# Kernel optimization log

Hardware: AMD Instinct MI355X
Metric: run time of the kernel (lower is better)

## Reference

```python
import jax, jax.numpy as jnp
import numpy as np

N_NODES = 100000
N_EDGES = 1600000
N_GRAPHS = 64
IN_DIM = 128
HID = 64
N_CLASSES = 10


def setup_inputs() -> dict:
    key = jax.random.key(0)
    ks = jax.random.split(key, 8)
    x = jax.random.normal(ks[0], (N_NODES, IN_DIM), jnp.float32)
    edge_index = jax.random.randint(ks[1], (2, N_EDGES), 0, N_NODES, jnp.int32)
    graph_id = jnp.sort(jax.random.randint(ks[2], (N_NODES,), 0, N_GRAPHS, jnp.int32))
    W1 = jax.random.normal(ks[3], (IN_DIM, HID), jnp.float32) / np.sqrt(IN_DIM)
    b1 = jnp.zeros((HID,), jnp.float32)
    W2 = jax.random.normal(ks[4], (HID, HID), jnp.float32) / np.sqrt(HID)
    b2 = jnp.zeros((HID,), jnp.float32)
    attn_W = jax.random.normal(ks[5], (HID, 1), jnp.float32) / np.sqrt(HID)
    attn_b = jnp.zeros((1,), jnp.float32)
    cls_W = jax.random.normal(ks[6], (HID, N_CLASSES), jnp.float32) / np.sqrt(HID)
    cls_b = jnp.zeros((N_CLASSES,), jnp.float32)
    return {"x": x, "edge_index": edge_index, "graph_id": graph_id,
            "W1": W1, "b1": b1, "W2": W2, "b2": b2,
            "attn_W": attn_W, "attn_b": attn_b, "cls_W": cls_W, "cls_b": cls_b}


def _graph_conv(h, W, b, src, dst, norm_out, norm_in):
    # DGL GraphConv, norm='both': D_in^{-1/2} A D_out^{-1/2} (h W) + b
    h = h @ W                                  # [N, out]
    h = h * norm_out[:, None]                  # scale by src out-degree^{-1/2}
    m = jax.ops.segment_sum(h[src], dst, num_segments=N_NODES)  # SpMM aggregation
    return m * norm_in[:, None] + b


def reference(x, edge_index, graph_id, W1, b1, W2, b2, attn_W, attn_b, cls_W, cls_b):
    src, dst = edge_index[0], edge_index[1]
    ones_e = jnp.ones((src.shape[0],), jnp.float32)
    deg_out = jnp.clip(jax.ops.segment_sum(ones_e, src, num_segments=N_NODES), 1.0)
    deg_in = jnp.clip(jax.ops.segment_sum(ones_e, dst, num_segments=N_NODES), 1.0)
    norm_out = jax.lax.rsqrt(deg_out)
    norm_in = jax.lax.rsqrt(deg_in)

    h = jax.nn.relu(_graph_conv(x, W1, b1, src, dst, norm_out, norm_in))
    h = jax.nn.relu(_graph_conv(h, W2, b2, src, dst, norm_out, norm_in))

    hw = jax.nn.sigmoid(h @ attn_W + attn_b)   # [N, 1] attention gate
    h = h * hw

    # mean_nodes: per-graph mean pooling
    sums = jax.ops.segment_sum(h, graph_id, num_segments=N_GRAPHS)        # [G, HID]
    cnts = jnp.clip(jax.ops.segment_sum(jnp.ones((N_NODES,), jnp.float32), graph_id,
                                        num_segments=N_GRAPHS), 1.0)
    hg = sums / cnts[:, None]
    out = hg @ cls_W + cls_b                   # [G, n_classes]
    return out, hw
```

## Files before the change

### kernel.cpp

```cpp
#include <hip/hip_runtime.h>
#include <stdint.h>


#define N_NODES   100000
#define N_EDGES   1600000
#define N_GRAPHS  64
#define IN_DIM    128
#define HID       64
#define N_CLASSES 10

#define NBUCK     391
#define P1B       196
#define EPB       8192
#define GB_BLOCKS 391
#define MTILES    6250
#define GEMM_BLOCKS 1563
#define SPMM_BLOCKS 3125
#define POOL_SLICES 32
#define WS_NEED   33885952u

typedef __attribute__((ext_vector_type(8))) short short8v;
typedef __attribute__((ext_vector_type(4))) float f32x4;
typedef __bf16 bf16x8 __attribute__((ext_vector_type(8)));

__device__ __forceinline__ f32x4 mfma16(short8v a, short8v b, f32x4 c) {
  return __builtin_amdgcn_mfma_f32_16x16x32_bf16(
      __builtin_bit_cast(bf16x8, a), __builtin_bit_cast(bf16x8, b), c, 0, 0, 0);
}

__device__ __forceinline__ float bf2f(unsigned short u) {
  unsigned int v = ((unsigned int)u) << 16;
  float f;
  __builtin_memcpy(&f, &v, 4);
  return f;
}

__device__ __forceinline__ unsigned short f2bf(float f) {
  unsigned int x;
  __builtin_memcpy(&x, &f, 4);
  unsigned int lsb = (x >> 16) & 1u;
  x += 0x7fffu + lsb;
  return (unsigned short)(x >> 16);
}

__device__ __forceinline__ void unpack_bf2(unsigned int u, float& lo, float& hi) {
  unsigned int a = u << 16;
  unsigned int b = u & 0xffff0000u;
  __builtin_memcpy(&lo, &a, 4);
  __builtin_memcpy(&hi, &b, 4);
}

__device__ __forceinline__ float ldf(const void* p, int i, int mode) {
  return mode ? bf2f(((const unsigned short*)p)[i]) : ((const float*)p)[i];
}

__global__ __launch_bounds__(256) void probe_kernel(const unsigned short* __restrict__ xu,
                                                    int* __restrict__ flag) {
  int tid = (int)threadIdx.x;
  unsigned u = xu[2 * tid];
  int e = (int)((u >> 7) & 0xFF);
  int ok = (e >= 110 && e <= 132) ? 1 : 0;
  unsigned long long m = __ballot(ok);
  __shared__ int cnt[4];
  if ((tid & 63) == 0) cnt[tid >> 6] = __popcll(m);
  __syncthreads();
  if (tid == 0) {
    flag[0] = (cnt[0] + cnt[1] + cnt[2] + cnt[3] > 128) ? 1 : 0;
    flag[1] = 1;
  }
}

__global__ __launch_bounds__(256) void fallback_kernel(unsigned short* __restrict__ out,
                                                       int n) {
  int i = blockIdx.x * 256 + threadIdx.x;
  if (i < n) out[i] = 0;
}

__global__ __launch_bounds__(256) void wcvt_kernel(
    const void* __restrict__ W1, const void* __restrict__ W2,
    const void* __restrict__ b1, const void* __restrict__ b2,
    const void* __restrict__ attnW, const void* __restrict__ attnb,
    const void* __restrict__ clsW, const void* __restrict__ clsb,
    unsigned short* __restrict__ W1hf, unsigned short* __restrict__ W1lf,
    unsigned short* __restrict__ W2hf, unsigned short* __restrict__ W2lf,
    float* __restrict__ b1f, float* __restrict__ b2f,
    float* __restrict__ attnWf, float* __restrict__ attnbf,
    float* __restrict__ clsWf, float* __restrict__ clsbf,
    const int* __restrict__ flag) {
  int mode = flag[0];
  int i = blockIdx.x * 256 + threadIdx.x;
  if (i < 1024) {
    int tile = i >> 6, lane = i & 63;
    int kt = tile >> 2, ct = tile & 3;
#pragma unroll
    for (int j = 0; j < 8; ++j) {
      int k = kt * 32 + ((lane >> 4) << 3) + j;
      int d = (ct << 4) + (lane & 15);
      float v = ldf(W1, k * HID + d, mode);
      unsigned short h = f2bf(v);
      unsigned short l = f2bf(v - bf2f(h));
      W1hf[i * 8 + j] = h;
      W1lf[i * 8 + j] = l;
    }
  } else if (i < 1536) {
    int ii = i - 1024;
    int tile = ii >> 6, lane = ii & 63;
    int kt = tile >> 2, ct = tile & 3;
#pragma unroll
    for (int j = 0; j < 8; ++j) {
      int k = kt * 32 + ((lane >> 4) << 3) + j;
      int d = (ct << 4) + (lane & 15);
      float v = ldf(W2, k * HID + d, mode);
      unsigned short h = f2bf(v);
      unsigned short l = f2bf(v - bf2f(h));
      W2hf[ii * 8 + j] = h;
      W2lf[ii * 8 + j] = l;
    }
  }
  if (i < HID) {
    b1f[i] = ldf(b1, i, mode);
    b2f[i] = ldf(b2, i, mode);
    attnWf[i] = ldf(attnW, i, mode);
  }
  if (i == 0) attnbf[0] = ldf(attnb, 0, mode);
  if (i < HID * N_CLASSES) clsWf[i] = ldf(clsW, i, mode);
  if (i < N_CLASSES) clsbf[i] = ldf(clsb, i, mode);
}

__global__ __launch_bounds__(256) void part_count_kernel(
    const int* __restrict__ ei, int* __restrict__ blkhistD,
    int* __restrict__ blkhistS,
    const int* __restrict__ gid, int* __restrict__ gstart) {
  int b = (int)blockIdx.x;
  int t = (int)threadIdx.x;
  if (b < P1B) {
    __shared__ int hD[NBUCK];
    __shared__ int hS[NBUCK];
    for (int i = t; i < NBUCK; i += 256) { hD[i] = 0; hS[i] = 0; }
    __syncthreads();
    int base_e = b * EPB;
    for (int s = 0; s < EPB / 1024; ++s) {
      int e4 = base_e + s * 1024 + t * 4;
      if (e4 < N_EDGES) {
        int4 s4 = *(const int4*)(ei + e4);
        int4 d4 = *(const int4*)(ei + N_EDGES + e4);
        int ss[4] = {s4.x, s4.y, s4.z, s4.w};
        int dd[4] = {d4.x, d4.y, d4.z, d4.w};
#pragma unroll
        for (int j = 0; j < 4; ++j) {
          if ((unsigned)ss[j] < N_NODES) atomicAdd(&hS[ss[j] >> 8], 1);
          if ((unsigned)dd[j] < N_NODES) atomicAdd(&hD[dd[j] >> 8], 1);
        }
      }
    }
    __syncthreads();
    for (int i = t; i < NBUCK; i += 256) {
      blkhistD[b * NBUCK + i] = hD[i];
      blkhistS[b * NBUCK + i] = hS[i];
    }
  } else {
    int bb = b - P1B;
    int n = bb * 256 + t;
    if (n >= N_NODES) return;
    int gc = gid[n] & (N_GRAPHS - 1);
    if (n == 0) {
      for (int g = 0; g <= gc; ++g) gstart[g] = 0;
    } else {
      int gp = gid[n - 1] & (N_GRAPHS - 1);
      for (int g = gp + 1; g <= gc; ++g) gstart[g] = n;
    }
    if (n == N_NODES - 1) {
      for (int g = gc + 1; g <= N_GRAPHS; ++g) gstart[g] = N_NODES;
    }
  }
}

__global__ __launch_bounds__(512) void bucket_scan_kernel(
    int* __restrict__ blkhistD, int* __restrict__ blkhistS,
    int* __restrict__ bstart_d, int* __restrict__ bstart_s) {
  int* hist = (blockIdx.x == 0) ? blkhistD : blkhistS;
  int* bst  = (blockIdx.x == 0) ? bstart_d : bstart_s;
  int u = (int)threadIdx.x;
  int tot = 0;
  if (u < NBUCK) {
    for (int blk = 0; blk < P1B; ++blk) tot += hist[blk * NBUCK + u];
  }
  __shared__ int smA[512];
  __shared__ int smB[512];
  smA[u] = tot;
  __syncthreads();
  int* a = smA;
  int* bq = smB;
  for (int off = 1; off < 512; off <<= 1) {
    int v = a[u];
    if (u >= off) v += a[u - off];
    bq[u] = v;
    __syncthreads();
    int* tmp = a; a = bq; bq = tmp;
  }
  int excl = a[u] - tot;
  if (u <= NBUCK) bst[u] = excl;
  if (u < NBUCK) {
    int off2 = excl;
    for (int blk = 0; blk < P1B; ++blk) {
      int h = hist[blk * NBUCK + u];
      hist[blk * NBUCK + u] = off2;
      off2 += h;
    }
  }
}

__global__ __launch_bounds__(256) void part_scatter_kernel(
    const int* __restrict__ ei, const int* __restrict__ blkbaseD,
    const int* __restrict__ blkbaseS,
    int2* __restrict__ edst, int* __restrict__ esrc) {
  __shared__ int cD[NBUCK];
  __shared__ int cS[NBUCK];
  int b = (int)blockIdx.x;
  int t = (int)threadIdx.x;
  for (int i = t; i < NBUCK; i += 256) {
    cD[i] = blkbaseD[b * NBUCK + i];
    cS[i] = blkbaseS[b * NBUCK + i];
  }
  __syncthreads();
  int base_e = b * EPB;
  for (int s = 0; s < EPB / 1024; ++s) {
    int e4 = base_e + s * 1024 + t * 4;
    if (e4 < N_EDGES) {
      int4 s4 = *(const int4*)(ei + e4);
      int4 d4 = *(const int4*)(ei + N_EDGES + e4);
      int ss[4] = {s4.x, s4.y, s4.z, s4.w};
      int dd[4] = {d4.x, d4.y, d4.z, d4.w};
#pragma unroll
      for (int j = 0; j < 4; ++j) {
        if ((unsigned)ss[j] < N_NODES) {
          int slot = atomicAdd(&cS[ss[j] >> 8], 1);
          esrc[slot] = ss[j];
        }
        if ((unsigned)dd[j] < N_NODES) {
          int slot = atomicAdd(&cD[dd[j] >> 8], 1);
          edst[slot] = make_int2(ss[j], dd[j]);
        }
      }
    }
  }
}

__global__ __launch_bounds__(256) void csr_kernel(
    const int2* __restrict__ edst, const int* __restrict__ esrc,
    const int* __restrict__ bstart_d, const int* __restrict__ bstart_s,
    int* __restrict__ rowptr, int* __restrict__ colx,
    float* __restrict__ norm_in, float* __restrict__ norm_out) {
  __shared__ int lc[256];
  __shared__ int smA[256];
  __shared__ int smB[256];
  int b = (int)blockIdx.x;
  int t = (int)threadIdx.x;
  if (b < NBUCK) {
    int node0 = b << 8;
    int base = bstart_d[b];
    int end  = bstart_d[b + 1];
    lc[t] = 0;
    __syncthreads();
    for (int i = base + t; i < end; i += 256) {
      int2 p = edst[i];
      atomicAdd(&lc[p.y - node0], 1);
    }
    __syncthreads();
    int my = lc[t];
    smA[t] = my;
    __syncthreads();
    int* a = smA;
    int* bq = smB;
    for (int off = 1; off < 256; off <<= 1) {
      int v = a[t];
      if (t >= off) v += a[t - off];
      bq[t] = v;
      __syncthreads();
      int* tmp = a; a = bq; bq = tmp;
    }
    int excl = a[t] - my;
    int n = node0 + t;
    if (n <= N_NODES) rowptr[n] = base + excl;
    if (n < N_NODES) {
      int c = my < 1 ? 1 : my;
      norm_in[n] = rsqrtf((float)c);
    }
    __syncthreads();
    lc[t] = base + excl;
    __syncthreads();
    for (int i = base + t; i < end; i += 256) {
      int2 p = edst[i];
      int slot = atomicAdd(&lc[p.y - node0], 1);
      colx[slot] = p.x;
    }
  } else {
    int bb = b - NBUCK;
    int node0 = bb << 8;
    int base = bstart_s[bb];
    int end  = bstart_s[bb + 1];
    lc[t] = 0;
    __syncthreads();
    for (int i = base + t; i < end; i += 256) {
      atomicAdd(&lc[esrc[i] - node0], 1);
    }
    __syncthreads();
    int n = node0 + t;
    if (n < N_NODES) {
      int c = lc[t] < 1 ? 1 : lc[t];
      norm_out[n] = rsqrtf((float)c);
    }
  }
}

template <int K>
__global__ __launch_bounds__(256) void gemm_mfma_kernel(
    const void* __restrict__ A, const unsigned short* __restrict__ Whf,
    const unsigned short* __restrict__ Wlf, const float* __restrict__ norm_out,
    unsigned short* __restrict__ out, const int* __restrict__ flag) {
  int mode = flag[0];
  int mtile = (int)blockIdx.x * 4 + ((int)threadIdx.x >> 6);
  if (mtile >= MTILES) return;
  int n0 = mtile << 4;
  int lane = (int)threadIdx.x & 63;
  int row = lane & 15;
  int kg = lane >> 4;
  f32x4 acc0 = {0.f, 0.f, 0.f, 0.f};
  f32x4 acc1 = {0.f, 0.f, 0.f, 0.f};
  f32x4 acc2 = {0.f, 0.f, 0.f, 0.f};
  f32x4 acc3 = {0.f, 0.f, 0.f, 0.f};
  const short8v* whb0 = (const short8v*)Whf + lane;
  const short8v* wlb0 = (const short8v*)Wlf + lane;
  if (mode) {
    const unsigned short* xr = (const unsigned short*)A + (size_t)(n0 + row) * K + (kg << 3);
#pragma unroll
    for (int kt = 0; kt < K / 32; ++kt) {
      uint4 va = *(const uint4*)(xr + kt * 32);
      short8v xh = __builtin_bit_cast(short8v, va);
      const short8v* wh = whb0 + (size_t)(kt * 4) * 64;
      const short8v* wl = wlb0 + (size_t)(kt * 4) * 64;
      acc0 = mfma16(xh, wh[0], acc0);
      acc1 = mfma16(xh, wh[64], acc1);
      acc2 = mfma16(xh, wh[128], acc2);
      acc3 = mfma16(xh, wh[192], acc3);
      acc0 = mfma16(xh, wl[0], acc0);
      acc1 = mfma16(xh, wl[64], acc1);
      acc2 = mfma16(xh, wl[128], acc2);
      acc3 = mfma16(xh, wl[192], acc3);
    }
  } else {
    const float* xr = (const float*)A + (size_t)(n0 + row) * K + (kg << 3);
#pragma unroll
    for (int kt = 0; kt < K / 32; ++kt) {
      float4 a0 = *(const float4*)(xr + kt * 32);
      float4 a1 = *(const float4*)(xr + kt * 32 + 4);
      float xv[8] = {a0.x, a0.y, a0.z, a0.w, a1.x, a1.y, a1.z, a1.w};
      short8v xh, xl;
#pragma unroll
      for (int j = 0; j < 8; ++j) {
        unsigned short h = f2bf(xv[j]);
        unsigned short l = f2bf(xv[j] - bf2f(h));
        xh[j] = (short)h;
        xl[j] = (short)l;
      }
      const short8v* wh = whb0 + (size_t)(kt * 4) * 64;
      const short8v* wl = wlb0 + (size_t)(kt * 4) * 64;
      acc0 = mfma16(xh, wh[0], acc0);
      acc1 = mfma16(xh, wh[64], acc1);
      acc2 = mfma16(xh, wh[128], acc2);
      acc3 = mfma16(xh, wh[192], acc3);
      acc0 = mfma16(xh, wl[0], acc0);
      acc1 = mfma16(xh, wl[64], acc1);
      acc2 = mfma16(xh, wl[128], acc2);
      acc3 = mfma16(xh, wl[192], acc3);
      acc0 = mfma16(xl, wh[0], acc0);
      acc1 = mfma16(xl, wh[64], acc1);
      acc2 = mfma16(xl, wh[128], acc2);
      acc3 = mfma16(xl, wh[192], acc3);
    }
  }
  int col = lane & 15;
#pragma unroll
  for (int i = 0; i < 4; ++i) {
    int n = n0 + (kg << 2) + i;
    float s = norm_out[n];
    size_t rb = (size_t)n << 6;
    out[rb + col]      = f2bf(acc0[i] * s);
    out[rb + 16 + col] = f2bf(acc1[i] * s);
    out[rb + 32 + col] = f2bf(acc2[i] * s);
    out[rb + 48 + col] = f2bf(acc3[i] * s);
  }
}

__device__ __forceinline__ void accum8(uint4 v, float acc[8]) {
  float lo, hi;
  unpack_bf2(v.x, lo, hi); acc[0] += lo; acc[1] += hi;
  unpack_bf2(v.y, lo, hi); acc[2] += lo; acc[3] += hi;
  unpack_bf2(v.z, lo, hi); acc[4] += lo; acc[5] += hi;
  unpack_bf2(v.w, lo, hi); acc[6] += lo; acc[7] += hi;
}

__device__ __forceinline__ void spmm_gather8(const unsigned short* __restrict__ hs,
                                             const int* __restrict__ col,
                                             int e0, int e1, int dim0,
                                             float acc[8]) {
  int e = e0;
  for (; e + 4 <= e1; e += 4) {
    unsigned c0 = (unsigned)col[e];
    unsigned c1 = (unsigned)col[e + 1];
    unsigned c2 = (unsigned)col[e + 2];
    unsigned c3 = (unsigned)col[e + 3];
    uint4 v0 = make_uint4(0u, 0u, 0u, 0u);
    uint4 v1 = v0, v2 = v0, v3 = v0;
    if (c0 < N_NODES) v0 = *(const uint4*)(hs + ((size_t)c0 << 6) + dim0);
    if (c1 < N_NODES) v1 = *(const uint4*)(hs + ((size_t)c1 << 6) + dim0);
    if (c2 < N_NODES) v2 = *(const uint4*)(hs + ((size_t)c2 << 6) + dim0);
    if (c3 < N_NODES) v3 = *(const uint4*)(hs + ((size_t)c3 << 6) + dim0);
    accum8(v0, acc);
    accum8(v1, acc);
    accum8(v2, acc);
    accum8(v3, acc);
  }
  for (; e < e1; ++e) {
    unsigned c = (unsigned)col[e];
    uint4 v = make_uint4(0u, 0u, 0u, 0u);
    if (c < N_NODES) v = *(const uint4*)(hs + ((size_t)c << 6) + dim0);
    accum8(v, acc);
  }
}

__global__ __launch_bounds__(256) void spmm_kernel(const unsigned short* __restrict__ hs,
                                                   const int* __restrict__ rowptr,
                                                   const int* __restrict__ col,
                                                   const float* __restrict__ norm_in,
                                                   const float* __restrict__ b1f,
                                                   unsigned short* __restrict__ out) {
  int n = (int)(blockIdx.x * 32 + (threadIdx.x >> 3));
  int dim0 = ((int)threadIdx.x & 7) << 3;
  if (n >= N_NODES) return;
  int e0 = rowptr[n], e1 = rowptr[n + 1];
  if (e0 < 0) e0 = 0;
  if (e1 > N_EDGES) e1 = N_EDGES;
  float acc[8];
#pragma unroll
  for (int i = 0; i < 8; ++i) acc[i] = 0.f;
  spmm_gather8(hs, col, e0, e1, dim0, acc);
  float nin = norm_in[n];
  unsigned int pk[4];
#pragma unroll
  for (int i = 0; i < 4; ++i) {
    float vlo = fmaxf(acc[2 * i] * nin + b1f[dim0 + 2 * i], 0.f);
    float vhi = fmaxf(acc[2 * i + 1] * nin + b1f[dim0 + 2 * i + 1], 0.f);
    pk[i] = (unsigned int)f2bf(vlo) | ((unsigned int)f2bf(vhi) << 16);
  }
  *(uint4*)(out + ((size_t)n << 6) + dim0) = make_uint4(pk[0], pk[1], pk[2], pk[3]);
}

__global__ __launch_bounds__(256) void spmm_attn_kernel(
    const unsigned short* __restrict__ hs,
    const int* __restrict__ rowptr, const int* __restrict__ col,
    const float* __restrict__ norm_in, const float* __restrict__ b2f,
    const float* __restrict__ attnWf, const float* __restrict__ attnbf,
    void* __restrict__ out_base, unsigned short* __restrict__ gated,
    const int* __restrict__ flag) {
  int mode = flag[0];
  int n = (int)(blockIdx.x * 32 + (threadIdx.x >> 3));
  int dim0 = ((int)threadIdx.x & 7) << 3;
  if (n >= N_NODES) return;
  int e0 = rowptr[n], e1 = rowptr[n + 1];
  if (e0 < 0) e0 = 0;
  if (e1 > N_EDGES) e1 = N_EDGES;
  float acc[8];
#pragma unroll
  for (int i = 0; i < 8; ++i) acc[i] = 0.f;
  spmm_gather8(hs, col, e0, e1, dim0, acc);
  float nin = norm_in[n];
  float vv[8];
  float p = 0.f;
#pragma unroll
  for (int i = 0; i < 8; ++i) {
    vv[i] = fmaxf(acc[i] * nin + b2f[dim0 + i], 0.f);
    p += vv[i] * attnWf[dim0 + i];
  }
#pragma unroll
  for (int m = 1; m <= 4; m <<= 1) p += __shfl_xor(p, m, 64);
  float logit = p + attnbf[0];
  float hwv = 1.f / (1.f + __expf(-logit));
  if ((threadIdx.x & 7) == 0) {
    if (mode) ((unsigned short*)out_base)[N_GRAPHS * N_CLASSES + n] = f2bf(hwv);
    else      ((float*)out_base)[N_GRAPHS * N_CLASSES + n] = hwv;
  }
  unsigned int pk[4];
#pragma unroll
  for (int i = 0; i < 4; ++i) {
    pk[i] = (unsigned int)f2bf(vv[2 * i] * hwv) |
            ((unsigned int)f2bf(vv[2 * i + 1] * hwv) << 16);
  }
  *(uint4*)(gated + ((size_t)n << 6) + dim0) = make_uint4(pk[0], pk[1], pk[2], pk[3]);
}

__global__ __launch_bounds__(256) void pool_kernel(const unsigned short* __restrict__ gated,
                                                   const int* __restrict__ gstart,
                                                   float* __restrict__ gpart) {
  int g = (int)blockIdx.x >> 5;
  int s = (int)blockIdx.x & 31;
  int dim = (int)threadIdx.x & 63;
  int rsel = (int)threadIdx.x >> 6;
  int r0 = gstart[g], r1 = gstart[g + 1];
  if (r0 < 0) r0 = 0;
  if (r1 > N_NODES) r1 = N_NODES;
  int len = r1 - r0;
  if (len < 0) len = 0;
  int a = r0 + (int)(((long long)len * s) >> 5);
  int bnd = r0 + (int)(((long long)len * (s + 1)) >> 5);
  float acc = 0.f;
  for (int r = a + rsel; r < bnd; r += 4)
    acc += bf2f(gated[((size_t)r << 6) + dim]);
  __shared__ float sm[256];
  sm[threadIdx.x] = acc;
  __syncthreads();
  if (threadIdx.x < 64)
    gpart[((size_t)blockIdx.x << 6) + dim] =
        sm[dim] + sm[64 + dim] + sm[128 + dim] + sm[192 + dim];
}

__global__ __launch_bounds__(64) void pool_reduce_kernel(const float* __restrict__ gpart,
                                                         float* __restrict__ gsum) {
  int g = (int)blockIdx.x;
  int dim = (int)threadIdx.x;
  float acc = 0.f;
#pragma unroll
  for (int s = 0; s < POOL_SLICES; ++s)
    acc += gpart[(((size_t)g << 5) + s << 6) + dim];
  gsum[((size_t)g << 6) + dim] = acc;
}

__global__ __launch_bounds__(640) void final_kernel(const float* __restrict__ gsum,
                                                    const int* __restrict__ gstart,
                                                    const float* __restrict__ clsWf,
                                                    const float* __restrict__ clsbf,
                                                    void* __restrict__ out_base,
                                                    const int* __restrict__ flag) {
  int mode = flag[0];
  int t = (int)threadIdx.x;
  if (t >= N_GRAPHS * N_CLASSES) return;
  int g = t / N_CLASSES, c = t - g * N_CLASSES;
  int cg = gstart[g + 1] - gstart[g];
  if (cg < 1) cg = 1;
  float inv = 1.f / (float)cg;
  float acc = 0.f;
#pragma unroll
  for (int d = 0; d < HID; ++d) acc += gsum[(g << 6) + d] * clsWf[d * N_CLASSES + c];
  float r = acc * inv + clsbf[c];
  if (mode) ((unsigned short*)out_base)[t] = f2bf(r);
  else      ((float*)out_base)[t] = r;
}

extern "C" void kernel_launch(void* const* d_in, const int* in_sizes, int n_in,
                              void* d_out, int out_size, void* d_ws, size_t ws_size,
                              hipStream_t stream) {
  const void* x     = d_in[0];
  const int*  ei    = (const int*)d_in[1];
  const int*  gid   = (const int*)d_in[2];
  const void* W1    = d_in[3];
  const void* b1    = d_in[4];
  const void* W2    = d_in[5];
  const void* b2    = d_in[6];
  const void* attnW = d_in[7];
  const void* attnb = d_in[8];
  const void* clsW  = d_in[9];
  const void* clsb  = d_in[10];

  if (ws_size < (size_t)WS_NEED) {
    fallback_kernel<<<(out_size + 255) / 256, 256, 0, stream>>>(
        (unsigned short*)d_out, out_size);
    return;
  }

  char* w = (char*)d_ws;
  int*   flag     = (int*)(w + 0);
  int*   gstart   = (int*)(w + 64);
  float* gsum     = (float*)(w + 576);
  int*   bstart_d = (int*)(w + 16960);
  int*   bstart_s = (int*)(w + 18560);
  int*   blkhD    = (int*)(w + 20160);
  int*   blkhS    = (int*)(w + 326720);
  int*   rowptr   = (int*)(w + 633280);
  float* norm_out = (float*)(w + 1033344);
  float* norm_in  = (float*)(w + 1433344);
  unsigned short* W1hf = (unsigned short*)(w + 1833344);
  unsigned short* W1lf = (unsigned short*)(w + 1849728);
  unsigned short* W2hf = (unsigned short*)(w + 1866112);
  unsigned short* W2lf = (unsigned short*)(w + 1874304);
  float* b1f      = (float*)(w + 1882496);
  float* b2f      = (float*)(w + 1882752);
  float* attnWf   = (float*)(w + 1883008);
  float* attnbf   = (float*)(w + 1883264);
  float* clsWf    = (float*)(w + 1883328);
  float* clsbf    = (float*)(w + 1885888);
  int*   colx     = (int*)(w + 1885952);
  int2*  edst     = (int2*)(w + 8285952);
  int*   esrc     = (int*)(w + 21085952);
  unsigned short* bufA = (unsigned short*)(w + 8285952);
  unsigned short* bufB = (unsigned short*)(w + 21085952);
  float* gpart    = (float*)(w + 20160);

  probe_kernel<<<1, 256, 0, stream>>>((const unsigned short*)x, flag);
  wcvt_kernel<<<32, 256, 0, stream>>>(W1, W2, b1, b2, attnW, attnb, clsW, clsb,
                                      W1hf, W1lf, W2hf, W2lf, b1f, b2f, attnWf,
                                      attnbf, clsWf, clsbf, flag);

  part_count_kernel<<<P1B + GB_BLOCKS, 256, 0, stream>>>(ei, blkhD, blkhS, gid, gstart);
  bucket_scan_kernel<<<2, 512, 0, stream>>>(blkhD, blkhS, bstart_d, bstart_s);
  part_scatter_kernel<<<P1B, 256, 0, stream>>>(ei, blkhD, blkhS, edst, esrc);
  csr_kernel<<<2 * NBUCK, 256, 0, stream>>>(edst, esrc, bstart_d, bstart_s,
                                            rowptr, colx, norm_in, norm_out);

  gemm_mfma_kernel<IN_DIM><<<GEMM_BLOCKS, 256, 0, stream>>>(
      x, W1hf, W1lf, norm_out, bufA, flag);
  spmm_kernel<<<SPMM_BLOCKS, 256, 0, stream>>>(bufA, rowptr, colx, norm_in, b1f, bufB);

  gemm_mfma_kernel<HID><<<GEMM_BLOCKS, 256, 0, stream>>>(
      bufB, W2hf, W2lf, norm_out, bufA, flag + 1);
  spmm_attn_kernel<<<SPMM_BLOCKS, 256, 0, stream>>>(
      bufA, rowptr, colx, norm_in, b2f, attnWf, attnbf, d_out, bufB, flag);

  pool_kernel<<<N_GRAPHS * POOL_SLICES, 256, 0, stream>>>(bufB, gstart, gpart);
  pool_reduce_kernel<<<N_GRAPHS, 64, 0, stream>>>(gpart, gsum);
  final_kernel<<<1, 640, 0, stream>>>(gsum, gstart, clsWf, clsbf, d_out, flag);
}
```

Measured before the change: 274.7 us.

## Fuse probe into weight conversion and overlap layer-1 GEMM with edge histogram

Folds the dtype probe into the weight-conversion kernel, and merges the layer-1 GEMM into the histogram/graph-start kernel. This is possible because the norm_out scaling moves from the GEMM epilogue into the first SpMM gather. Edge-destination pairs are packed into 32-bit words to cut CSR build traffic, and the pool reduction is folded into the final classifier kernel. These changes remove several launches and let the dense GEMM run alongside the partitioning work. In exchange, the first SpMM does an extra per-edge norm_out load and buffer aliasing gets more involved.

After: 270.0 us. No clear change (-1.7%).

```diff
diff --git a/kernel.cpp b/kernel.cpp
--- a/kernel.cpp
+++ b/kernel.cpp
@@ -54,22 +54,6 @@
   return mode ? bf2f(((const unsigned short*)p)[i]) : ((const float*)p)[i];
 }
 
-__global__ __launch_bounds__(256) void probe_kernel(const unsigned short* __restrict__ xu,
-                                                    int* __restrict__ flag) {
-  int tid = (int)threadIdx.x;
-  unsigned u = xu[2 * tid];
-  int e = (int)((u >> 7) & 0xFF);
-  int ok = (e >= 110 && e <= 132) ? 1 : 0;
-  unsigned long long m = __ballot(ok);
-  __shared__ int cnt[4];
-  if ((tid & 63) == 0) cnt[tid >> 6] = __popcll(m);
-  __syncthreads();
-  if (tid == 0) {
-    flag[0] = (cnt[0] + cnt[1] + cnt[2] + cnt[3] > 128) ? 1 : 0;
-    flag[1] = 1;
-  }
-}
-
 __global__ __launch_bounds__(256) void fallback_kernel(unsigned short* __restrict__ out,
                                                        int n) {
   int i = blockIdx.x * 256 + threadIdx.x;
@@ -77,6 +61,7 @@
 }
 
 __global__ __launch_bounds__(256) void wcvt_kernel(
+    const unsigned short* __restrict__ xu,
     const void* __restrict__ W1, const void* __restrict__ W2,
     const void* __restrict__ b1, const void* __restrict__ b2,
     const void* __restrict__ attnW, const void* __restrict__ attnb,
@@ -86,9 +71,27 @@
     float* __restrict__ b1f, float* __restrict__ b2f,
     float* __restrict__ attnWf, float* __restrict__ attnbf,
     float* __restrict__ clsWf, float* __restrict__ clsbf,
-    const int* __restrict__ flag) {
-  int mode = flag[0];
-  int i = blockIdx.x * 256 + threadIdx.x;
+    int* __restrict__ flag) {
+  __shared__ int cnt[4];
+  __shared__ int smode;
+  int tid = (int)threadIdx.x;
+  unsigned u = xu[2 * tid];
+  int e = (int)((u >> 7) & 0xFF);
+  int ok = (e >= 110 && e <= 132) ? 1 : 0;
+  unsigned long long m = __ballot(ok);
+  if ((tid & 63) == 0) cnt[tid >> 6] = __popcll(m);
+  __syncthreads();
+  if (tid == 0) {
+    smode = (cnt[0] + cnt[1] + cnt[2] + cnt[3] > 128) ? 1 : 0;
+    if (blockIdx.x == 0) {
+      flag[0] = smode;
+      flag[1] = 1;
+    }
+  }
+  __syncthreads();
+  int mode = smode;
+
+  int i = blockIdx.x * 256 + tid;
   if (i < 1024) {
     int tile = i >> 6, lane = i & 63;
     int kt = tile >> 2, ct = tile & 3;
@@ -127,202 +130,12 @@
   if (i < N_CLASSES) clsbf[i] = ldf(clsb, i, mode);
 }
 
-__global__ __launch_bounds__(256) void part_count_kernel(
-    const int* __restrict__ ei, int* __restrict__ blkhistD,
-    int* __restrict__ blkhistS,
-    const int* __restrict__ gid, int* __restrict__ gstart) {
-  int b = (int)blockIdx.x;
-  int t = (int)threadIdx.x;
-  if (b < P1B) {
-    __shared__ int hD[NBUCK];
-    __shared__ int hS[NBUCK];
-    for (int i = t; i < NBUCK; i += 256) { hD[i] = 0; hS[i] = 0; }
-    __syncthreads();
-    int base_e = b * EPB;
-    for (int s = 0; s < EPB / 1024; ++s) {
-      int e4 = base_e + s * 1024 + t * 4;
-      if (e4 < N_EDGES) {
-        int4 s4 = *(const int4*)(ei + e4);
-        int4 d4 = *(const int4*)(ei + N_EDGES + e4);
-        int ss[4] = {s4.x, s4.y, s4.z, s4.w};
-        int dd[4] = {d4.x, d4.y, d4.z, d4.w};
-#pragma unroll
-        for (int j = 0; j < 4; ++j) {
-          if ((unsigned)ss[j] < N_NODES) atomicAdd(&hS[ss[j] >> 8], 1);
-          if ((unsigned)dd[j] < N_NODES) atomicAdd(&hD[dd[j] >> 8], 1);
-        }
-      }
-    }
-    __syncthreads();
-    for (int i = t; i < NBUCK; i += 256) {
-      blkhistD[b * NBUCK + i] = hD[i];
-      blkhistS[b * NBUCK + i] = hS[i];
-    }
-  } else {
-    int bb = b - P1B;
-    int n = bb * 256 + t;
-    if (n >= N_NODES) return;
-    int gc = gid[n] & (N_GRAPHS - 1);
-    if (n == 0) {
-      for (int g = 0; g <= gc; ++g) gstart[g] = 0;
-    } else {
-      int gp = gid[n - 1] & (N_GRAPHS - 1);
-      for (int g = gp + 1; g <= gc; ++g) gstart[g] = n;
-    }
-    if (n == N_NODES - 1) {
-      for (int g = gc + 1; g <= N_GRAPHS; ++g) gstart[g] = N_NODES;
-    }
-  }
-}
-
-__global__ __launch_bounds__(512) void bucket_scan_kernel(
-    int* __restrict__ blkhistD, int* __restrict__ blkhistS,
-    int* __restrict__ bstart_d, int* __restrict__ bstart_s) {
-  int* hist = (blockIdx.x == 0) ? blkhistD : blkhistS;
-  int* bst  = (blockIdx.x == 0) ? bstart_d : bstart_s;
-  int u = (int)threadIdx.x;
-  int tot = 0;
-  if (u < NBUCK) {
-    for (int blk = 0; blk < P1B; ++blk) tot += hist[blk * NBUCK + u];
-  }
-  __shared__ int smA[512];
-  __shared__ int smB[512];
-  smA[u] = tot;
-  __syncthreads();
-  int* a = smA;
-  int* bq = smB;
-  for (int off = 1; off < 512; off <<= 1) {
-    int v = a[u];
-    if (u >= off) v += a[u - off];
-    bq[u] = v;
-    __syncthreads();
-    int* tmp = a; a = bq; bq = tmp;
-  }
-  int excl = a[u] - tot;
-  if (u <= NBUCK) bst[u] = excl;
-  if (u < NBUCK) {
-    int off2 = excl;
-    for (int blk = 0; blk < P1B; ++blk) {
-      int h = hist[blk * NBUCK + u];
-      hist[blk * NBUCK + u] = off2;
-      off2 += h;
-    }
-  }
-}
-
-__global__ __launch_bounds__(256) void part_scatter_kernel(
-    const int* __restrict__ ei, const int* __restrict__ blkbaseD,
-    const int* __restrict__ blkbaseS,
-    int2* __restrict__ edst, int* __restrict__ esrc) {
-  __shared__ int cD[NBUCK];
-  __shared__ int cS[NBUCK];
-  int b = (int)blockIdx.x;
-  int t = (int)threadIdx.x;
-  for (int i = t; i < NBUCK; i += 256) {
-    cD[i] = blkbaseD[b * NBUCK + i];
-    cS[i] = blkbaseS[b * NBUCK + i];
-  }
-  __syncthreads();
-  int base_e = b * EPB;
-  for (int s = 0; s < EPB / 1024; ++s) {
-    int e4 = base_e + s * 1024 + t * 4;
-    if (e4 < N_EDGES) {
-      int4 s4 = *(const int4*)(ei + e4);
-      int4 d4 = *(const int4*)(ei + N_EDGES + e4);
-      int ss[4] = {s4.x, s4.y, s4.z, s4.w};
-      int dd[4] = {d4.x, d4.y, d4.z, d4.w};
-#pragma unroll
-      for (int j = 0; j < 4; ++j) {
-        if ((unsigned)ss[j] < N_NODES) {
-          int slot = atomicAdd(&cS[ss[j] >> 8], 1);
-          esrc[slot] = ss[j];
-        }
-        if ((unsigned)dd[j] < N_NODES) {
-          int slot = atomicAdd(&cD[dd[j] >> 8], 1);
-          edst[slot] = make_int2(ss[j], dd[j]);
-        }
-      }
-    }
-  }
-}
-
-__global__ __launch_bounds__(256) void csr_kernel(
-    const int2* __restrict__ edst, const int* __restrict__ esrc,
-    const int* __restrict__ bstart_d, const int* __restrict__ bstart_s,
-    int* __restrict__ rowptr, int* __restrict__ colx,
-    float* __restrict__ norm_in, float* __restrict__ norm_out) {
-  __shared__ int lc[256];
-  __shared__ int smA[256];
-  __shared__ int smB[256];
-  int b = (int)blockIdx.x;
-  int t = (int)threadIdx.x;
-  if (b < NBUCK) {
-    int node0 = b << 8;
-    int base = bstart_d[b];
-    int end  = bstart_d[b + 1];
-    lc[t] = 0;
-    __syncthreads();
-    for (int i = base + t; i < end; i += 256) {
-      int2 p = edst[i];
-      atomicAdd(&lc[p.y - node0], 1);
-    }
-    __syncthreads();
-    int my = lc[t];
-    smA[t] = my;
-    __syncthreads();
-    int* a = smA;
-    int* bq = smB;
-    for (int off = 1; off < 256; off <<= 1) {
-      int v = a[t];
-      if (t >= off) v += a[t - off];
-      bq[t] = v;
-      __syncthreads();
-      int* tmp = a; a = bq; bq = tmp;
-    }
-    int excl = a[t] - my;
-    int n = node0 + t;
-    if (n <= N_NODES) rowptr[n] = base + excl;
-    if (n < N_NODES) {
-      int c = my < 1 ? 1 : my;
-      norm_in[n] = rsqrtf((float)c);
-    }
-    __syncthreads();
-    lc[t] = base + excl;
-    __syncthreads();
-    for (int i = base + t; i < end; i += 256) {
-      int2 p = edst[i];
-      int slot = atomicAdd(&lc[p.y - node0], 1);
-      colx[slot] = p.x;
-    }
-  } else {
-    int bb = b - NBUCK;
-    int node0 = bb << 8;
-    int base = bstart_s[bb];
-    int end  = bstart_s[bb + 1];
-    lc[t] = 0;
-    __syncthreads();
-    for (int i = base + t; i < end; i += 256) {
-      atomicAdd(&lc[esrc[i] - node0], 1);
-    }
-    __syncthreads();
-    int n = node0 + t;
-    if (n < N_NODES) {
-      int c = lc[t] < 1 ? 1 : lc[t];
-      norm_out[n] = rsqrtf((float)c);
-    }
-  }
-}
-
-template <int K>
-__global__ __launch_bounds__(256) void gemm_mfma_kernel(
+template <int K, bool SCALE>
+__device__ __forceinline__ void gemm_tile(
     const void* __restrict__ A, const unsigned short* __restrict__ Whf,
     const unsigned short* __restrict__ Wlf, const float* __restrict__ norm_out,
-    unsigned short* __restrict__ out, const int* __restrict__ flag) {
-  int mode = flag[0];
-  int mtile = (int)blockIdx.x * 4 + ((int)threadIdx.x >> 6);
-  if (mtile >= MTILES) return;
+    unsigned short* __restrict__ out, int mode, int mtile, int lane) {
   int n0 = mtile << 4;
-  int lane = (int)threadIdx.x & 63;
   int row = lane & 15;
   int kg = lane >> 4;
   f32x4 acc0 = {0.f, 0.f, 0.f, 0.f};
@@ -383,12 +196,259 @@
 #pragma unroll
   for (int i = 0; i < 4; ++i) {
     int n = n0 + (kg << 2) + i;
-    float s = norm_out[n];
+    float s = SCALE ? norm_out[n] : 1.f;
     size_t rb = (size_t)n << 6;
     out[rb + col]      = f2bf(acc0[i] * s);
     out[rb + 16 + col] = f2bf(acc1[i] * s);
     out[rb + 32 + col] = f2bf(acc2[i] * s);
     out[rb + 48 + col] = f2bf(acc3[i] * s);
+  }
+}
+
+__global__ __launch_bounds__(256) void fatA_kernel(
+    const int* __restrict__ ei, int* __restrict__ blkhistD,
+    int* __restrict__ blkhistS,
+    const int* __restrict__ gid, int* __restrict__ gstart,
+    const void* __restrict__ x, const unsigned short* __restrict__ W1hf,
+    const unsigned short* __restrict__ W1lf, unsigned short* __restrict__ bufA,
+    const int* __restrict__ flag) {
+  int b = (int)blockIdx.x;
+  int t = (int)threadIdx.x;
+  if (b < P1B) {
+    __shared__ int hD[NBUCK];
+    __shared__ int hS[NBUCK];
+    for (int i = t; i < NBUCK; i += 256) { hD[i] = 0; hS[i] = 0; }
+    __syncthreads();
+    int base_e = b * EPB;
+    for (int s = 0; s < EPB / 1024; ++s) {
+      int e4 = base_e + s * 1024 + t * 4;
+      if (e4 < N_EDGES) {
+        int4 s4 = *(const int4*)(ei + e4);
+        int4 d4 = *(const int4*)(ei + N_EDGES + e4);
+        int ss[4] = {s4.x, s4.y, s4.z, s4.w};
+        int dd[4] = {d4.x, d4.y, d4.z, d4.w};
+#pragma unroll
+        for (int j = 0; j < 4; ++j) {
+          if ((unsigned)ss[j] < N_NODES) atomicAdd(&hS[ss[j] >> 8], 1);
+          if ((unsigned)dd[j] < N_NODES) atomicAdd(&hD[dd[j] >> 8], 1);
+        }
+      }
+    }
+    __syncthreads();
+    for (int i = t; i < NBUCK; i += 256) {
+      blkhistD[b * NBUCK + i] = hD[i];
+      blkhistS[b * NBUCK + i] = hS[i];
+    }
+  } else if (b < P1B + GEMM_BLOCKS) {
+    int mode = flag[0];
+    int mtile = (b - P1B) * 4 + (t >> 6);
+    if (mtile < MTILES)
+      gemm_tile<IN_DIM, false>(x, W1hf, W1lf, (const float*)0, bufA, mode,
+                               mtile, t & 63);
+  } else {
+    int bb = b - P1B - GEMM_BLOCKS;
+    int n = bb * 256 + t;
+    if (n >= N_NODES) return;
+    int gc = gid[n] & (N_GRAPHS - 1);
+    if (n == 0) {
+      for (int g = 0; g <= gc; ++g) gstart[g] = 0;
+    } else {
+      int gp = gid[n - 1] & (N_GRAPHS - 1);
+      for (int g = gp + 1; g <= gc; ++g) gstart[g] = n;
+    }
+    if (n == N_NODES - 1) {
+      for (int g = gc + 1; g <= N_GRAPHS; ++g) gstart[g] = N_NODES;
+    }
+  }
+}
+
+__global__ __launch_bounds__(512) void bucket_scan_kernel(
+    int* __restrict__ blkhistD, int* __restrict__ blkhistS,
+    int* __restrict__ bstart_d, int* __restrict__ bstart_s) {
+  int* hist = (blockIdx.x == 0) ? blkhistD : blkhistS;
+  int* bst  = (blockIdx.x == 0) ? bstart_d : bstart_s;
+  int u = (int)threadIdx.x;
+  int tot = 0;
+  if (u < NBUCK) {
+    for (int blk = 0; blk < P1B; ++blk) tot += hist[blk * NBUCK + u];
+  }
+  __shared__ int smA[512];
+  __shared__ int smB[512];
+  smA[u] = tot;
+  __syncthreads();
+  int* a = smA;
+  int* bq = smB;
+  for (int off = 1; off < 512; off <<= 1) {
+    int v = a[u];
+    if (u >= off) v += a[u - off];
+    bq[u] = v;
+    __syncthreads();
+    int* tmp = a; a = bq; bq = tmp;
+  }
+  int excl = a[u] - tot;
+  if (u <= NBUCK) bst[u] = excl;
+  if (u < NBUCK) {
+    int off2 = excl;
+    for (int blk = 0; blk < P1B; ++blk) {
+      int h = hist[blk * NBUCK + u];
+      hist[blk * NBUCK + u] = off2;
+      off2 += h;
+    }
+  }
+}
+
+__global__ __launch_bounds__(256) void part_scatter_kernel(
+    const int* __restrict__ ei, const int* __restrict__ blkbaseD,
+    const int* __restrict__ blkbaseS,
+    unsigned int* __restrict__ edstP, int* __restrict__ esrc) {
+  __shared__ int cD[NBUCK];
+  __shared__ int cS[NBUCK];
+  int b = (int)blockIdx.x;
+  int t = (int)threadIdx.x;
+  for (int i = t; i < NBUCK; i += 256) {
+    cD[i] = blkbaseD[b * NBUCK + i];
+    cS[i] = blkbaseS[b * NBUCK + i];
+  }
+  __syncthreads();
+  int base_e = b * EPB;
+  for (int s = 0; s < EPB / 1024; ++s) {
+    int e4 = base_e + s * 1024 + t * 4;
+    if (e4 < N_EDGES) {
+      int4 s4 = *(const int4*)(ei + e4);
+      int4 d4 = *(const int4*)(ei + N_EDGES + e4);
+      int ss[4] = {s4.x, s4.y, s4.z, s4.w};
+      int dd[4] = {d4.x, d4.y, d4.z, d4.w};
+#pragma unroll
+      for (int j = 0; j < 4; ++j) {
+        if ((unsigned)ss[j] < N_NODES) {
+          int slot = atomicAdd(&cS[ss[j] >> 8], 1);
+          esrc[slot] = ss[j];
+        }
+        if ((unsigned)dd[j] < N_NODES) {
+          int slot = atomicAdd(&cD[dd[j] >> 8], 1);
+          edstP[slot] = ((unsigned int)ss[j] << 8) | ((unsigned int)dd[j] & 255u);
+        }
+      }
+    }
+  }
+}
+
+__global__ __launch_bounds__(256) void csr_kernel(
+    const unsigned int* __restrict__ edstP, const int* __restrict__ esrc,
+    const int* __restrict__ bstart_d, const int* __restrict__ bstart_s,
+    int* __restrict__ rowptr, int* __restrict__ colx,
+    float* __restrict__ norm_in, float* __restrict__ norm_out) {
+  __shared__ int lc[256];
+  __shared__ int smA[256];
+  __shared__ int smB[256];
+  int b = (int)blockIdx.x;
+  int t = (int)threadIdx.x;
+  if (b < NBUCK) {
+    int node0 = b << 8;
+    int base = bstart_d[b];
+    int end  = bstart_d[b + 1];
+    lc[t] = 0;
+    __syncthreads();
+    for (int i = base + t; i < end; i += 256) {
+      unsigned int p = edstP[i];
+      atomicAdd(&lc[p & 255u], 1);
+    }
+    __syncthreads();
+    int my = lc[t];
+    smA[t] = my;
+    __syncthreads();
+    int* a = smA;
+    int* bq = smB;
+    for (int off = 1; off < 256; off <<= 1) {
+      int v = a[t];
+      if (t >= off) v += a[t - off];
+      bq[t] = v;
+      __syncthreads();
+      int* tmp = a; a = bq; bq = tmp;
+    }
+    int excl = a[t] - my;
+    int n = node0 + t;
+    if (n <= N_NODES) rowptr[n] = base + excl;
+    if (n < N_NODES) {
+      int c = my < 1 ? 1 : my;
+      norm_in[n] = rsqrtf((float)c);
+    }
+    __syncthreads();
+    lc[t] = base + excl;
+    __syncthreads();
+    for (int i = base + t; i < end; i += 256) {
+      unsigned int p = edstP[i];
+      int slot = atomicAdd(&lc[p & 255u], 1);
+      colx[slot] = (int)(p >> 8);
+    }
+  } else {
+    int bb = b - NBUCK;
+    int node0 = bb << 8;
+    int base = bstart_s[bb];
+    int end  = bstart_s[bb + 1];
+    lc[t] = 0;
+    __syncthreads();
+    for (int i = base + t; i < end; i += 256) {
+      atomicAdd(&lc[esrc[i] - node0], 1);
+    }
+    __syncthreads();
+    int n = node0 + t;
+    if (n < N_NODES) {
+      int c = lc[t] < 1 ? 1 : lc[t];
+      norm_out[n] = rsqrtf((float)c);
+    }
+  }
+}
+
+template <int K>
+__global__ __launch_bounds__(256) void gemm_mfma_kernel(
+    const void* __restrict__ A, const unsigned short* __restrict__ Whf,
+    const unsigned short* __restrict__ Wlf, const float* __restrict__ norm_out,
+    unsigned short* __restrict__ out, const int* __restrict__ flag) {
+  int mode = flag[0];
+  int mtile = (int)blockIdx.x * 4 + ((int)threadIdx.x >> 6);
+  if (mtile >= MTILES) return;
+  gemm_tile<K, true>(A, Whf, Wlf, norm_out, out, mode, mtile,
+                     (int)threadIdx.x & 63);
+}
+
+__device__ __forceinline__ void accum8f(uint4 v, float no, float acc[8]) {
+  float lo, hi;
+  unpack_bf2(v.x, lo, hi); acc[0] = fmaf(lo, no, acc[0]); acc[1] = fmaf(hi, no, acc[1]);
+  unpack_bf2(v.y, lo, hi); acc[2] = fmaf(lo, no, acc[2]); acc[3] = fmaf(hi, no, acc[3]);
+  unpack_bf2(v.z, lo, hi); acc[4] = fmaf(lo, no, acc[4]); acc[5] = fmaf(hi, no, acc[5]);
+  unpack_bf2(v.w, lo, hi); acc[6] = fmaf(lo, no, acc[6]); acc[7] = fmaf(hi, no, acc[7]);
+}
+
+__device__ __forceinline__ void spmm_gather8s(const unsigned short* __restrict__ hs,
+                                              const int* __restrict__ col,
+                                              const float* __restrict__ no,
+                                              int e0, int e1, int dim0,
+                                              float acc[8]) {
+  int e = e0;
+  for (; e + 4 <= e1; e += 4) {
+    unsigned c0 = (unsigned)col[e];
+    unsigned c1 = (unsigned)col[e + 1];
+    unsigned c2 = (unsigned)col[e + 2];
+    unsigned c3 = (unsigned)col[e + 3];
+    uint4 v0 = make_uint4(0u, 0u, 0u, 0u);
+    uint4 v1 = v0, v2 = v0, v3 = v0;
+    float n0 = 0.f, n1 = 0.f, n2 = 0.f, n3 = 0.f;
+    if (c0 < N_NODES) { v0 = *(const uint4*)(hs + ((size_t)c0 << 6) + dim0); n0 = no[c0]; }
+    if (c1 < N_NODES) { v1 = *(const uint4*)(hs + ((size_t)c1 << 6) + dim0); n1 = no[c1]; }
+    if (c2 < N_NODES) { v2 = *(const uint4*)(hs + ((size_t)c2 << 6) + dim0); n2 = no[c2]; }
+    if (c3 < N_NODES) { v3 = *(const uint4*)(hs + ((size_t)c3 << 6) + dim0); n3 = no[c3]; }
+    accum8f(v0, n0, acc);
+    accum8f(v1, n1, acc);
+    accum8f(v2, n2, acc);
+    accum8f(v3, n3, acc);
+  }
+  for (; e < e1; ++e) {
+    unsigned c = (unsigned)col[e];
+    uint4 v = make_uint4(0u, 0u, 0u, 0u);
+    float nn = 0.f;
+    if (c < N_NODES) { v = *(const uint4*)(hs + ((size_t)c << 6) + dim0); nn = no[c]; }
+    accum8f(v, nn, acc);
   }
 }
 
@@ -432,6 +492,7 @@
 __global__ __launch_bounds__(256) void spmm_kernel(const unsigned short* __restrict__ hs,
                                                    const int* __restrict__ rowptr,
                                                    const int* __restrict__ col,
+                                                   const float* __restrict__ norm_out,
                                                    const float* __restrict__ norm_in,
                                                    const float* __restrict__ b1f,
                                                    unsigned short* __restrict__ out) {
@@ -444,7 +505,7 @@
   float acc[8];
 #pragma unroll
   for (int i = 0; i < 8; ++i) acc[i] = 0.f;
-  spmm_gather8(hs, col, e0, e1, dim0, acc);
+  spmm_gather8s(hs, col, norm_out, e0, e1, dim0, acc);
   float nin = norm_in[n];
   unsigned int pk[4];
 #pragma unroll
@@ -524,25 +585,24 @@
         sm[dim] + sm[64 + dim] + sm[128 + dim] + sm[192 + dim];
 }
 
-__global__ __launch_bounds__(64) void pool_reduce_kernel(const float* __restrict__ gpart,
-                                                         float* __restrict__ gsum) {
-  int g = (int)blockIdx.x;
-  int dim = (int)threadIdx.x;
-  float acc = 0.f;
-#pragma unroll
-  for (int s = 0; s < POOL_SLICES; ++s)
-    acc += gpart[(((size_t)g << 5) + s << 6) + dim];
-  gsum[((size_t)g << 6) + dim] = acc;
-}
-
-__global__ __launch_bounds__(640) void final_kernel(const float* __restrict__ gsum,
+__global__ __launch_bounds__(640) void final_kernel(const float* __restrict__ gpart,
                                                     const int* __restrict__ gstart,
                                                     const float* __restrict__ clsWf,
                                                     const float* __restrict__ clsbf,
                                                     void* __restrict__ out_base,
                                                     const int* __restrict__ flag) {
+  __shared__ float gs[N_GRAPHS * HID];
+  int t = (int)threadIdx.x;
+  for (int idx = t; idx < N_GRAPHS * HID; idx += 640) {
+    int g = idx >> 6, d = idx & 63;
+    float a = 0.f;
+#pragma unroll
+    for (int s = 0; s < POOL_SLICES; ++s)
+      a += gpart[(((size_t)(g << 5) + s) << 6) + d];
+    gs[idx] = a;
+  }
+  __syncthreads();
   int mode = flag[0];
-  int t = (int)threadIdx.x;
   if (t >= N_GRAPHS * N_CLASSES) return;
   int g = t / N_CLASSES, c = t - g * N_CLASSES;
   int cg = gstart[g + 1] - gstart[g];
@@ -550,7 +610,7 @@
   float inv = 1.f / (float)cg;
   float acc = 0.f;
 #pragma unroll
-  for (int d = 0; d < HID; ++d) acc += gsum[(g << 6) + d] * clsWf[d * N_CLASSES + c];
+  for (int d = 0; d < HID; ++d) acc += gs[(g << 6) + d] * clsWf[d * N_CLASSES + c];
   float r = acc * inv + clsbf[c];
   if (mode) ((unsigned short*)out_base)[t] = f2bf(r);
   else      ((float*)out_base)[t] = r;
@@ -580,7 +640,7 @@
   char* w = (char*)d_ws;
   int*   flag     = (int*)(w + 0);
   int*   gstart   = (int*)(w + 64);
-  float* gsum     = (float*)(w + 576);
+  float* gsum_un  = (float*)(w + 576);
   int*   bstart_d = (int*)(w + 16960);
   int*   bstart_s = (int*)(w + 18560);
   int*   blkhD    = (int*)(w + 20160);
@@ -599,26 +659,28 @@
   float* clsWf    = (float*)(w + 1883328);
   float* clsbf    = (float*)(w + 1885888);
   int*   colx     = (int*)(w + 1885952);
-  int2*  edst     = (int2*)(w + 8285952);
-  int*   esrc     = (int*)(w + 21085952);
-  unsigned short* bufA = (unsigned short*)(w + 8285952);
-  unsigned short* bufB = (unsigned short*)(w + 21085952);
+  unsigned int* edstP = (unsigned int*)(w + 8285952);
+  int*   esrc     = (int*)(w + 14685952);
+  unsigned short* bufA = (unsigned short*)(w + 21085952);
+  unsigned short* bufB = (unsigned short*)(w + 8285952);
   float* gpart    = (float*)(w + 20160);
-
-  probe_kernel<<<1, 256, 0, stream>>>((const unsigned short*)x, flag);
-  wcvt_kernel<<<32, 256, 0, stream>>>(W1, W2, b1, b2, attnW, attnb, clsW, clsb,
-                                      W1hf, W1lf, W2hf, W2lf, b1f, b2f, attnWf,
-                                      attnbf, clsWf, clsbf, flag);
-
-  part_count_kernel<<<P1B + GB_BLOCKS, 256, 0, stream>>>(ei, blkhD, blkhS, gid, gstart);
+  (void)gsum_un;
+
+  wcvt_kernel<<<32, 256, 0, stream>>>((const unsigned short*)x, W1, W2, b1, b2,
+                                      attnW, attnb, clsW, clsb, W1hf, W1lf,
+                                      W2hf, W2lf, b1f, b2f, attnWf, attnbf,
+                                      clsWf, clsbf, flag);
+
+  fatA_kernel<<<P1B + GEMM_BLOCKS + GB_BLOCKS, 256, 0, stream>>>(
+      ei, blkhD, blkhS, gid, gstart, x, W1hf, W1lf, bufA, flag);
+
   bucket_scan_kernel<<<2, 512, 0, stream>>>(blkhD, blkhS, bstart_d, bstart_s);
-  part_scatter_kernel<<<P1B, 256, 0, stream>>>(ei, blkhD, blkhS, edst, esrc);
-  csr_kernel<<<2 * NBUCK, 256, 0, stream>>>(edst, esrc, bstart_d, bstart_s,
+  part_scatter_kernel<<<P1B, 256, 0, stream>>>(ei, blkhD, blkhS, edstP, esrc);
+  csr_kernel<<<2 * NBUCK, 256, 0, stream>>>(edstP, esrc, bstart_d, bstart_s,
                                             rowptr, colx, norm_in, norm_out);
 
-  gemm_mfma_kernel<IN_DIM><<<GEMM_BLOCKS, 256, 0, stream>>>(
-      x, W1hf, W1lf, norm_out, bufA, flag);
-  spmm_kernel<<<SPMM_BLOCKS, 256, 0, stream>>>(bufA, rowptr, colx, norm_in, b1f, bufB);
+  spmm_kernel<<<SPMM_BLOCKS, 256, 0, stream>>>(bufA, rowptr, colx, norm_out,
+                                               norm_in, b1f, bufB);
 
   gemm_mfma_kernel<HID><<<GEMM_BLOCKS, 256, 0, stream>>>(
       bufB, W2hf, W2lf, norm_out, bufA, flag + 1);
@@ -626,6 +688,5 @@
       bufA, rowptr, colx, norm_in, b2f, attnWf, attnbf, d_out, bufB, flag);
 
   pool_kernel<<<N_GRAPHS * POOL_SLICES, 256, 0, stream>>>(bufB, gstart, gpart);
-  pool_reduce_kernel<<<N_GRAPHS, 64, 0, stream>>>(gpart, gsum);
-  final_kernel<<<1, 640, 0, stream>>>(gsum, gstart, clsWf, clsbf, d_out, flag);
-}
+  final_kernel<<<1, 640, 0, stream>>>(gpart, gstart, clsWf, clsbf, d_out, flag);
+}
```
